# Performance work log

Measured on AMD Instinct MI355X. Metric: run time of the kernel, lower is better.

Reference implementation:

```python
import jax, jax.numpy as jnp
import numpy as np

NUM_SAMPLES = 2048
MAX_AGENTS = 64
D_MODEL = 128
NUM_HEADS = 8


def setup_inputs() -> dict:
    key = jax.random.key(0)
    # deterministic ragged sizes: 1..64 repeating -> total = 32 * (64*65/2) = 66560
    agents = ((np.arange(NUM_SAMPLES) % MAX_AGENTS) + 1).astype(np.int32)
    total = int(agents.sum())
    k1, k2, k3 = jax.random.split(key, 3)
    s = 1.0 / np.sqrt(D_MODEL)
    return {
        "att_in": jax.random.normal(k1, (total, D_MODEL), jnp.float32),
        "in_proj_w": jax.random.uniform(k2, (3 * D_MODEL, D_MODEL), jnp.float32, -s, s),
        "in_proj_b": jnp.zeros((3 * D_MODEL,), jnp.float32),
        "out_proj_w": jax.random.uniform(k3, (D_MODEL, D_MODEL), jnp.float32, -s, s),
        "out_proj_b": jnp.zeros((D_MODEL,), jnp.float32),
        "agents_per_sample": jnp.asarray(agents),
    }


def reference(att_in, in_proj_w, in_proj_b, out_proj_w, out_proj_b, agents_per_sample):
    # agents_per_sample is static ragged metadata (host ints)
    agents = np.asarray(agents_per_sample)
    B = len(agents)
    A = int(agents.max())
    D = att_in.shape[-1]
    hd = D // NUM_HEADS

    # scatter ragged tokens into zero-padded [B, A, D]
    sample_ids = np.repeat(np.arange(B), agents)
    pos = np.concatenate([np.arange(n) for n in agents])
    padded = jnp.zeros((B, A, D), att_in.dtype).at[sample_ids, pos].set(att_in)
    key_valid = jnp.asarray(np.arange(A)[None, :] < agents[:, None])  # [B, A]

    # torch nn.MultiheadAttention math (eval mode, dropout=0)
    qkv = padded @ in_proj_w.T + in_proj_b  # [B, A, 3D]
    q, k, v = jnp.split(qkv, 3, axis=-1)
    q = q.reshape(B, A, NUM_HEADS, hd)
    k = k.reshape(B, A, NUM_HEADS, hd)
    v = v.reshape(B, A, NUM_HEADS, hd)

    scores = jnp.einsum("bqhd,bkhd->bhqk", q, k) / jnp.sqrt(jnp.asarray(hd, q.dtype))
    scores = jnp.where(key_valid[:, None, None, :], scores, jnp.asarray(-1e30, scores.dtype))
    attn = jax.nn.softmax(scores, axis=-1)

    out = jnp.einsum("bhqk,bkhd->bqhd", attn, v).reshape(B, A, D)
    out = out @ out_proj_w.T + out_proj_b

    # unpad: concatenation of the per-sample ragged outputs
    return out[sample_ids, pos]
```

## Files before the change

### kernel.cpp

```cpp
#include <hip/hip_runtime.h>

#define DM 128
#define NHEADS 8

typedef __attribute__((ext_vector_type(8))) __bf16 bf16x8;
typedef __attribute__((ext_vector_type(8))) unsigned short u16x8;
typedef __attribute__((ext_vector_type(4))) float f32x4;

__device__ inline unsigned short f2bf(float f) {
    unsigned u = __float_as_uint(f);
    u += 0x7FFFu + ((u >> 16) & 1u);
    return (unsigned short)(u >> 16);
}

__global__ void prep(const int* __restrict__ agents, int B,
                     const float* __restrict__ wqkv, const float* __restrict__ wout,
                     int* __restrict__ offs,
                     unsigned short* __restrict__ wqkv_bf,
                     unsigned short* __restrict__ wout_bf) {
    if (blockIdx.x < 64) {
        int idx = (blockIdx.x * 256 + threadIdx.x) * 4;
        if (idx < 49152) {
            float4 v = *(const float4*)(wqkv + idx);
            ushort4 o;
            o.x = f2bf(v.x); o.y = f2bf(v.y); o.z = f2bf(v.z); o.w = f2bf(v.w);
            *(ushort4*)(wqkv_bf + idx) = o;
        } else {
            int j = idx - 49152;
            float4 v = *(const float4*)(wout + j);
            ushort4 o;
            o.x = f2bf(v.x); o.y = f2bf(v.y); o.z = f2bf(v.z); o.w = f2bf(v.w);
            *(ushort4*)(wout_bf + j) = o;
        }
    } else {
        __shared__ int part[256];
        const int tid = threadIdx.x;
        const int per = (B + 255) >> 8;
        const int base = tid * per;
        int s = 0;
        for (int i = 0; i < per; ++i) {
            int idx = base + i;
            if (idx < B) s += agents[idx];
        }
        part[tid] = s;
        __syncthreads();
        for (int off = 1; off < 256; off <<= 1) {
            int v = (tid >= off) ? part[tid - off] : 0;
            __syncthreads();
            part[tid] += v;
            __syncthreads();
        }
        int run = (tid == 0) ? 0 : part[tid - 1];
        for (int i = 0; i < per; ++i) {
            int idx = base + i;
            if (idx < B) { offs[idx] = run; run += agents[idx]; }
        }
    }
}

template<int NT>
__device__ __forceinline__ void fused_body(
    const unsigned short* __restrict__ wqkvb, const float* __restrict__ bqkv,
    const unsigned short* __restrict__ woutb, const float* __restrict__ bout,
    float* __restrict__ out,
    unsigned short* __restrict__ Xs, unsigned short* __restrict__ Vs,
    int n, int base, int h, int quad, int l16)
{
    constexpr int G   = (NT + 1) / 2;
    constexpr int KT2 = 2 * G;
    bf16x8 qf[NT], kf[NT];
    const int shA = (quad & 1) * 32 + l16;
    const int shB = shA + 16;

    #pragma unroll
    for (int seg = 0; seg < 3; ++seg) {
        bf16x8 wf[4];
        #pragma unroll
        for (int ks = 0; ks < 4; ++ks)
            wf[ks] = *(const bf16x8*)(wqkvb +
                     (size_t)(seg * 128 + h * 16 + l16) * 128 + ks * 32 + quad * 8);
        const float4 bs = *(const float4*)(bqkv + seg * 128 + h * 16 + quad * 4);
        #pragma unroll
        for (int mt = 0; mt < NT; ++mt) {
            f32x4 acc = {0.f, 0.f, 0.f, 0.f};
            #pragma unroll
            for (int ks = 0; ks < 4; ++ks) {
                bf16x8 xf = *(const bf16x8*)&Xs[(mt * 16 + l16) * 136 + ks * 32 + quad * 8];
                acc = __builtin_amdgcn_mfma_f32_16x16x32_bf16(wf[ks], xf, acc, 0, 0, 0);
            }
            ushort4 w;
            w.x = f2bf(acc[0] + bs.x); w.y = f2bf(acc[1] + bs.y);
            w.z = f2bf(acc[2] + bs.z); w.w = f2bf(acc[3] + bs.w);
            if (seg == 2) {
                *(ushort4*)&Vs[(mt * 16 + l16) * 136 + h * 16 + quad * 4] = w;
            } else {
                unsigned u0 = (unsigned)w.x | ((unsigned)w.y << 16);
                unsigned u1 = (unsigned)w.z | ((unsigned)w.w << 16);
                uint4 q;
                q.x = __shfl(u0, shA); q.y = __shfl(u1, shA);
                q.z = __shfl(u0, shB); q.w = __shfl(u1, shB);
                bf16x8 fr = (quad < 2) ? __builtin_bit_cast(bf16x8, q)
                                       : (bf16x8)(__bf16)0.0f;
                if (seg == 0) qf[mt] = fr; else kf[mt] = fr;
            }
        }
    }

    bf16x8 vA[G];
    const __bf16* Vsb = (const __bf16*)Vs;
    #pragma unroll
    for (int g = 0; g < G; ++g)
        #pragma unroll
        for (int j = 0; j < 8; ++j)
            vA[g][j] = Vsb[(size_t)(g * 32 + ((j >> 2) * 16) + quad * 4 + (j & 3)) * 136
                           + h * 16 + l16];

    __syncthreads();

    int thr[KT2];
    #pragma unroll
    for (int kt = 0; kt < KT2; ++kt) {
        int t = n - kt * 16 - quad * 4;
        thr[kt] = t < 0 ? 0 : (t > 4 ? 4 : t);
    }
    const float SC2 = 0.25f * 1.44269504088896340736f;
    unsigned short* Os = Xs;

    #pragma unroll
    for (int mt = 0; mt < NT; ++mt) {
        float pr[KT2][4];
        float mm = -3.0e38f;
        #pragma unroll
        for (int kt = 0; kt < KT2; ++kt) {
            if (kt < NT) {
                f32x4 sc = __builtin_amdgcn_mfma_f32_16x16x32_bf16(
                    kf[kt], qf[mt], (f32x4){0.f, 0.f, 0.f, 0.f}, 0, 0, 0);
                #pragma unroll
                for (int r = 0; r < 4; ++r) {
                    float v = sc[r] * SC2;
                    pr[kt][r] = v;
                    mm = fmaxf(mm, v);
                }
            } else {
                #pragma unroll
                for (int r = 0; r < 4; ++r) pr[kt][r] = -3.0e38f;
            }
        }
        mm = fmaxf(mm, __shfl_xor(mm, 16));
        mm = fmaxf(mm, __shfl_xor(mm, 32));
        float ll = 0.f;
        #pragma unroll
        for (int kt = 0; kt < KT2; ++kt)
            #pragma unroll
            for (int r = 0; r < 4; ++r) {
                float e = exp2f(pr[kt][r] - mm);
                e = (r < thr[kt]) ? e : 0.f;
                pr[kt][r] = e;
                ll += e;
            }
        ll += __shfl_xor(ll, 16);
        ll += __shfl_xor(ll, 32);
        float inv = __builtin_amdgcn_rcpf(ll);
        bf16x8 pf[G];
        #pragma unroll
        for (int g = 0; g < G; ++g)
            #pragma unroll
            for (int j = 0; j < 8; ++j)
                pf[g][j] = (__bf16)(pr[2 * g + (j >> 2)][j & 3] * inv);
        f32x4 o = __builtin_amdgcn_mfma_f32_16x16x32_bf16(
            vA[0], pf[0], (f32x4){0.f, 0.f, 0.f, 0.f}, 0, 0, 0);
        if constexpr (G == 2)
            o = __builtin_amdgcn_mfma_f32_16x16x32_bf16(vA[1], pf[1], o, 0, 0, 0);
        const int row = mt * 16 + l16;
        if (row < n) {
            ushort4 w;
            w.x = f2bf(o[0]); w.y = f2bf(o[1]); w.z = f2bf(o[2]); w.w = f2bf(o[3]);
            *(ushort4*)&Os[row * 136 + h * 16 + quad * 4] = w;
        }
    }
    __syncthreads();

    bf16x8 wf2[4];
    #pragma unroll
    for (int ks = 0; ks < 4; ++ks)
        wf2[ks] = *(const bf16x8*)(woutb +
                  (size_t)(h * 16 + l16) * 128 + ks * 32 + quad * 8);
    const float4 bo = *(const float4*)(bout + h * 16 + quad * 4);
    #pragma unroll
    for (int mt = 0; mt < NT; ++mt) {
        const int row = mt * 16 + l16;
        f32x4 acc = {0.f, 0.f, 0.f, 0.f};
        #pragma unroll
        for (int ks = 0; ks < 4; ++ks) {
            bf16x8 af = *(const bf16x8*)&Os[row * 136 + ks * 32 + quad * 8];
            acc = __builtin_amdgcn_mfma_f32_16x16x32_bf16(wf2[ks], af, acc, 0, 0, 0);
        }
        if (row < n) {
            float4 o;
            o.x = acc[0] + bo.x; o.y = acc[1] + bo.y;
            o.z = acc[2] + bo.z; o.w = acc[3] + bo.w;
            *(float4*)(out + (size_t)(base + row) * DM + h * 16 + quad * 4) = o;
        }
    }
}

#define XS_OFF 0
#define VS_OFF 17408
#define SMEMF  34816

__launch_bounds__(512, 4)
__global__ void fused(const float* __restrict__ x,
                      const unsigned short* __restrict__ wqkvb,
                      const float* __restrict__ bqkv,
                      const unsigned short* __restrict__ woutb,
                      const float* __restrict__ bout,
                      float* __restrict__ out,
                      const int* __restrict__ agents,
                      const int* __restrict__ offs) {
    __shared__ __align__(16) char smem[SMEMF];
    unsigned short* Xs = (unsigned short*)(smem + XS_OFF);
    unsigned short* Vs = (unsigned short*)(smem + VS_OFF);

    const int s = blockIdx.x;
    const int n = agents[s];
    const int base = offs[s];
    const int tid = threadIdx.x;
    const int h = tid >> 6, lane = tid & 63, quad = lane >> 4, l16 = lane & 15;

    for (int f = tid; f < 1088; f += 512)
        ((uint4*)(smem + VS_OFF))[f] = make_uint4(0u, 0u, 0u, 0u);
    for (int f = tid; f < 2048; f += 512) {
        int t = f >> 5, c = f & 31;
        ushort4 o = make_ushort4(0, 0, 0, 0);
        if (t < n) {
            float4 v = *(const float4*)(x + (size_t)(base + t) * DM + c * 4);
            o.x = f2bf(v.x); o.y = f2bf(v.y); o.z = f2bf(v.z); o.w = f2bf(v.w);
        }
        *(ushort4*)&Xs[t * 136 + c * 4] = o;
    }
    __syncthreads();

    const int nkt = (n + 15) >> 4;
    if      (nkt == 1) fused_body<1>(wqkvb, bqkv, woutb, bout, out, Xs, Vs, n, base, h, quad, l16);
    else if (nkt == 2) fused_body<2>(wqkvb, bqkv, woutb, bout, out, Xs, Vs, n, base, h, quad, l16);
    else if (nkt == 3) fused_body<3>(wqkvb, bqkv, woutb, bout, out, Xs, Vs, n, base, h, quad, l16);
    else               fused_body<4>(wqkvb, bqkv, woutb, bout, out, Xs, Vs, n, base, h, quad, l16);
}

extern "C" void kernel_launch(void* const* d_in, const int* in_sizes, int n_in,
                              void* d_out, int out_size, void* d_ws, size_t ws_size,
                              hipStream_t stream) {
    const float* att_in     = (const float*)d_in[0];
    const float* in_proj_w  = (const float*)d_in[1];
    const float* in_proj_b  = (const float*)d_in[2];
    const float* out_proj_w = (const float*)d_in[3];
    const float* out_proj_b = (const float*)d_in[4];
    const int*   agents     = (const int*)d_in[5];
    const int B = in_sizes[5];

    int* offs = (int*)d_ws;
    unsigned short* wqkv_bf = (unsigned short*)((char*)d_ws + 8192);
    unsigned short* wout_bf = (unsigned short*)((char*)d_ws + 106496);

    hipLaunchKernelGGL(prep, dim3(65), dim3(256), 0, stream,
                       agents, B, in_proj_w, out_proj_w, offs, wqkv_bf, wout_bf);
    hipLaunchKernelGGL(fused, dim3(B), dim3(512), 0, stream,
                       att_in, wqkv_bf, in_proj_b, wout_bf, out_proj_b,
                       (float*)d_out, agents, offs);
}
```

Measured before the change: 149.0 us.

## Split fused attention into bf16 pre-conversion, QKV-attention, and output-projection kernels

Moves the fp32-to-bf16 conversion of the input tokens into the prep kernel. The per-sample kernel now reads bf16 rows straight from global memory and keeps V in registers through a swapped-operand MFMA, so it needs no shared-memory staging. The attention output goes to a global bf16 buffer that reuses the input buffer in place. A separate tiled kernel then does the output projection with the weights staged in LDS. The aim is to cut LDS use and synchronisation in the per-sample kernel and to run the projection as a dense GEMM, at the cost of an extra launch and extra global round trips.

```diff
diff --git a/kernel.cpp b/kernel.cpp
--- a/kernel.cpp
+++ b/kernel.cpp
@@ -1,10 +1,8 @@
 #include <hip/hip_runtime.h>
 
 #define DM 128
-#define NHEADS 8
 
 typedef __attribute__((ext_vector_type(8))) __bf16 bf16x8;
-typedef __attribute__((ext_vector_type(8))) unsigned short u16x8;
 typedef __attribute__((ext_vector_type(4))) float f32x4;
 
 __device__ inline unsigned short f2bf(float f) {
@@ -13,11 +11,13 @@
     return (unsigned short)(u >> 16);
 }
 
-__global__ void prep(const int* __restrict__ agents, int B,
+__global__ void prep(const int* __restrict__ agents, int B, int M,
                      const float* __restrict__ wqkv, const float* __restrict__ wout,
+                     const float* __restrict__ x,
                      int* __restrict__ offs,
                      unsigned short* __restrict__ wqkv_bf,
-                     unsigned short* __restrict__ wout_bf) {
+                     unsigned short* __restrict__ wout_bf,
+                     unsigned short* __restrict__ xbf) {
     if (blockIdx.x < 64) {
         int idx = (blockIdx.x * 256 + threadIdx.x) * 4;
         if (idx < 49152) {
@@ -32,7 +32,7 @@
             o.x = f2bf(v.x); o.y = f2bf(v.y); o.z = f2bf(v.z); o.w = f2bf(v.w);
             *(ushort4*)(wout_bf + j) = o;
         }
-    } else {
+    } else if (blockIdx.x == 64) {
         __shared__ int part[256];
         const int tid = threadIdx.x;
         const int per = (B + 255) >> 8;
@@ -55,25 +55,38 @@
             int idx = base + i;
             if (idx < B) { offs[idx] = run; run += agents[idx]; }
         }
+    } else {
+        const int nf4 = M * 32;
+        const int stride = ((int)gridDim.x - 65) * 256;
+        for (int idx = ((int)blockIdx.x - 65) * 256 + (int)threadIdx.x; idx < nf4;
+             idx += stride) {
+            float4 v = ((const float4*)x)[idx];
+            ushort4 o;
+            o.x = f2bf(v.x); o.y = f2bf(v.y); o.z = f2bf(v.z); o.w = f2bf(v.w);
+            ((ushort4*)xbf)[idx] = o;
+        }
     }
 }
 
 template<int NT>
-__device__ __forceinline__ void fused_body(
-    const unsigned short* __restrict__ wqkvb, const float* __restrict__ bqkv,
-    const unsigned short* __restrict__ woutb, const float* __restrict__ bout,
-    float* __restrict__ out,
-    unsigned short* __restrict__ Xs, unsigned short* __restrict__ Vs,
-    int n, int base, int h, int quad, int l16)
+__device__ __forceinline__ void qa_body(
+    const unsigned short* __restrict__ xbf,
+    const unsigned short* __restrict__ wqkvb,
+    const float* __restrict__ bqkv,
+    unsigned short* __restrict__ obuf,
+    int n, int base, int M, int h, int quad, int l16)
 {
     constexpr int G   = (NT + 1) / 2;
     constexpr int KT2 = 2 * G;
-    bf16x8 qf[NT], kf[NT];
+    bf16x8 qf[NT], kf[NT], vA[G];
+    #pragma unroll
+    for (int g = 0; g < G; ++g) vA[g] = (bf16x8)(__bf16)0.0f;
+
     const int shA = (quad & 1) * 32 + l16;
     const int shB = shA + 16;
 
     #pragma unroll
-    for (int seg = 0; seg < 3; ++seg) {
+    for (int seg = 0; seg < 2; ++seg) {
         bf16x8 wf[4];
         #pragma unroll
         for (int ks = 0; ks < 4; ++ks)
@@ -82,38 +95,51 @@
         const float4 bs = *(const float4*)(bqkv + seg * 128 + h * 16 + quad * 4);
         #pragma unroll
         for (int mt = 0; mt < NT; ++mt) {
+            int row = base + mt * 16 + l16;
+            row = row < M ? row : M - 1;
+            const unsigned short* xr = xbf + (size_t)row * 128;
             f32x4 acc = {0.f, 0.f, 0.f, 0.f};
             #pragma unroll
             for (int ks = 0; ks < 4; ++ks) {
-                bf16x8 xf = *(const bf16x8*)&Xs[(mt * 16 + l16) * 136 + ks * 32 + quad * 8];
+                bf16x8 xf = *(const bf16x8*)(xr + ks * 32 + quad * 8);
                 acc = __builtin_amdgcn_mfma_f32_16x16x32_bf16(wf[ks], xf, acc, 0, 0, 0);
             }
             ushort4 w;
             w.x = f2bf(acc[0] + bs.x); w.y = f2bf(acc[1] + bs.y);
             w.z = f2bf(acc[2] + bs.z); w.w = f2bf(acc[3] + bs.w);
-            if (seg == 2) {
-                *(ushort4*)&Vs[(mt * 16 + l16) * 136 + h * 16 + quad * 4] = w;
-            } else {
-                unsigned u0 = (unsigned)w.x | ((unsigned)w.y << 16);
-                unsigned u1 = (unsigned)w.z | ((unsigned)w.w << 16);
-                uint4 q;
-                q.x = __shfl(u0, shA); q.y = __shfl(u1, shA);
-                q.z = __shfl(u0, shB); q.w = __shfl(u1, shB);
-                bf16x8 fr = (quad < 2) ? __builtin_bit_cast(bf16x8, q)
-                                       : (bf16x8)(__bf16)0.0f;
-                if (seg == 0) qf[mt] = fr; else kf[mt] = fr;
+            unsigned u0 = (unsigned)w.x | ((unsigned)w.y << 16);
+            unsigned u1 = (unsigned)w.z | ((unsigned)w.w << 16);
+            uint4 q;
+            q.x = __shfl(u0, shA); q.y = __shfl(u1, shA);
+            q.z = __shfl(u0, shB); q.w = __shfl(u1, shB);
+            bf16x8 fr = (quad < 2) ? __builtin_bit_cast(bf16x8, q)
+                                   : (bf16x8)(__bf16)0.0f;
+            if (seg == 0) qf[mt] = fr; else kf[mt] = fr;
+        }
+    }
+    {
+        bf16x8 wfv[4];
+        #pragma unroll
+        for (int ks = 0; ks < 4; ++ks)
+            wfv[ks] = *(const bf16x8*)(wqkvb +
+                      (size_t)(256 + h * 16 + l16) * 128 + ks * 32 + quad * 8);
+        const float bv = bqkv[256 + h * 16 + l16];
+        #pragma unroll
+        for (int t = 0; t < NT; ++t) {
+            int row = base + t * 16 + l16;
+            row = row < M ? row : M - 1;
+            const unsigned short* xr = xbf + (size_t)row * 128;
+            f32x4 acc = {0.f, 0.f, 0.f, 0.f};
+            #pragma unroll
+            for (int ks = 0; ks < 4; ++ks) {
+                bf16x8 xf = *(const bf16x8*)(xr + ks * 32 + quad * 8);
+                acc = __builtin_amdgcn_mfma_f32_16x16x32_bf16(xf, wfv[ks], acc, 0, 0, 0);
             }
-        }
-    }
-
-    bf16x8 vA[G];
-    const __bf16* Vsb = (const __bf16*)Vs;
-    #pragma unroll
-    for (int g = 0; g < G; ++g)
-        #pragma unroll
-        for (int j = 0; j < 8; ++j)
-            vA[g][j] = Vsb[(size_t)(g * 32 + ((j >> 2) * 16) + quad * 4 + (j & 3)) * 136
-                           + h * 16 + l16];
+            #pragma unroll
+            for (int r = 0; r < 4; ++r)
+                vA[t >> 1][(t & 1) * 4 + r] = (__bf16)(acc[r] + bv);
+        }
+    }
 
     __syncthreads();
 
@@ -124,7 +150,6 @@
         thr[kt] = t < 0 ? 0 : (t > 4 ? 4 : t);
     }
     const float SC2 = 0.25f * 1.44269504088896340736f;
-    unsigned short* Os = Xs;
 
     #pragma unroll
     for (int mt = 0; mt < NT; ++mt) {
@@ -175,76 +200,78 @@
         if (row < n) {
             ushort4 w;
             w.x = f2bf(o[0]); w.y = f2bf(o[1]); w.z = f2bf(o[2]); w.w = f2bf(o[3]);
-            *(ushort4*)&Os[row * 136 + h * 16 + quad * 4] = w;
-        }
-    }
-    __syncthreads();
-
-    bf16x8 wf2[4];
-    #pragma unroll
-    for (int ks = 0; ks < 4; ++ks)
-        wf2[ks] = *(const bf16x8*)(woutb +
-                  (size_t)(h * 16 + l16) * 128 + ks * 32 + quad * 8);
-    const float4 bo = *(const float4*)(bout + h * 16 + quad * 4);
-    #pragma unroll
-    for (int mt = 0; mt < NT; ++mt) {
-        const int row = mt * 16 + l16;
-        f32x4 acc = {0.f, 0.f, 0.f, 0.f};
-        #pragma unroll
-        for (int ks = 0; ks < 4; ++ks) {
-            bf16x8 af = *(const bf16x8*)&Os[row * 136 + ks * 32 + quad * 8];
-            acc = __builtin_amdgcn_mfma_f32_16x16x32_bf16(wf2[ks], af, acc, 0, 0, 0);
-        }
-        if (row < n) {
-            float4 o;
-            o.x = acc[0] + bo.x; o.y = acc[1] + bo.y;
-            o.z = acc[2] + bo.z; o.w = acc[3] + bo.w;
-            *(float4*)(out + (size_t)(base + row) * DM + h * 16 + quad * 4) = o;
-        }
-    }
-}
-
-#define XS_OFF 0
-#define VS_OFF 17408
-#define SMEMF  34816
-
-__launch_bounds__(512, 4)
-__global__ void fused(const float* __restrict__ x,
-                      const unsigned short* __restrict__ wqkvb,
-                      const float* __restrict__ bqkv,
-                      const unsigned short* __restrict__ woutb,
-                      const float* __restrict__ bout,
-                      float* __restrict__ out,
-                      const int* __restrict__ agents,
-                      const int* __restrict__ offs) {
-    __shared__ __align__(16) char smem[SMEMF];
-    unsigned short* Xs = (unsigned short*)(smem + XS_OFF);
-    unsigned short* Vs = (unsigned short*)(smem + VS_OFF);
-
+            *(ushort4*)(obuf + (size_t)(base + row) * 128 + h * 16 + quad * 4) = w;
+        }
+    }
+}
+
+__launch_bounds__(512, 2)
+__global__ void qkvattn(const unsigned short* __restrict__ xbf,
+                        const unsigned short* __restrict__ wqkvb,
+                        const float* __restrict__ bqkv,
+                        unsigned short* __restrict__ obuf,
+                        const int* __restrict__ agents,
+                        const int* __restrict__ offs,
+                        int M) {
     const int s = blockIdx.x;
     const int n = agents[s];
     const int base = offs[s];
     const int tid = threadIdx.x;
-    const int h = tid >> 6, lane = tid & 63, quad = lane >> 4, l16 = lane & 15;
-
-    for (int f = tid; f < 1088; f += 512)
-        ((uint4*)(smem + VS_OFF))[f] = make_uint4(0u, 0u, 0u, 0u);
-    for (int f = tid; f < 2048; f += 512) {
-        int t = f >> 5, c = f & 31;
-        ushort4 o = make_ushort4(0, 0, 0, 0);
-        if (t < n) {
-            float4 v = *(const float4*)(x + (size_t)(base + t) * DM + c * 4);
-            o.x = f2bf(v.x); o.y = f2bf(v.y); o.z = f2bf(v.z); o.w = f2bf(v.w);
-        }
-        *(ushort4*)&Xs[t * 136 + c * 4] = o;
-    }
+    const int h = tid >> 6, quad = (tid >> 4) & 3, l16 = tid & 15;
+    const int nt = (n + 15) >> 4;
+    if      (nt == 1) qa_body<1>(xbf, wqkvb, bqkv, obuf, n, base, M, h, quad, l16);
+    else if (nt == 2) qa_body<2>(xbf, wqkvb, bqkv, obuf, n, base, M, h, quad, l16);
+    else if (nt == 3) qa_body<3>(xbf, wqkvb, bqkv, obuf, n, base, M, h, quad, l16);
+    else              qa_body<4>(xbf, wqkvb, bqkv, obuf, n, base, M, h, quad, l16);
+}
+
+__launch_bounds__(256, 4)
+__global__ void oproj(const unsigned short* __restrict__ attn_b,
+                      const unsigned short* __restrict__ woutb,
+                      const float* __restrict__ bout,
+                      float* __restrict__ out, int M) {
+    __shared__ __align__(16) unsigned short Ws[128 * 136];
+    __shared__ __align__(16) float biass[128];
+    const int m0 = blockIdx.x * 64;
+    const int tid = threadIdx.x;
+
+    for (int f = tid; f < 2048; f += 256) {
+        int t = f >> 4, c = f & 15;
+        *(uint4*)&Ws[t * 136 + c * 8] = *(const uint4*)(woutb + (size_t)t * 128 + c * 8);
+    }
+    if (tid < 32)
+        ((float4*)biass)[tid] = ((const float4*)bout)[tid];
     __syncthreads();
 
-    const int nkt = (n + 15) >> 4;
-    if      (nkt == 1) fused_body<1>(wqkvb, bqkv, woutb, bout, out, Xs, Vs, n, base, h, quad, l16);
-    else if (nkt == 2) fused_body<2>(wqkvb, bqkv, woutb, bout, out, Xs, Vs, n, base, h, quad, l16);
-    else if (nkt == 3) fused_body<3>(wqkvb, bqkv, woutb, bout, out, Xs, Vs, n, base, h, quad, l16);
-    else               fused_body<4>(wqkvb, bqkv, woutb, bout, out, Xs, Vs, n, base, h, quad, l16);
+    const int wave = tid >> 6, lane = tid & 63, quad = lane >> 4, l16 = lane & 15;
+    const int mw = m0 + wave * 16;
+
+    bf16x8 af[4];
+    {
+        int row = mw + l16;
+        row = (row < M) ? row : (M - 1);
+        #pragma unroll
+        for (int ks = 0; ks < 4; ++ks)
+            af[ks] = *(const bf16x8*)(attn_b + (size_t)row * DM + ks * 32 + quad * 8);
+    }
+
+    const int row0 = mw + l16;
+
+    for (int ct = 0; ct < 8; ++ct) {
+        bf16x8 bc[4];
+        #pragma unroll
+        for (int ks = 0; ks < 4; ++ks)
+            bc[ks] = *(const bf16x8*)&Ws[(ct * 16 + l16) * 136 + ks * 32 + quad * 8];
+        f32x4 a0 = {0.f, 0.f, 0.f, 0.f};
+        #pragma unroll
+        for (int ks = 0; ks < 4; ++ks)
+            a0 = __builtin_amdgcn_mfma_f32_16x16x32_bf16(bc[ks], af[ks], a0, 0, 0, 0);
+        const int n0 = ct * 16 + quad * 4;
+        const float4 b4 = *(const float4*)(biass + n0);
+        float4 o0;
+        o0.x = a0[0] + b4.x; o0.y = a0[1] + b4.y; o0.z = a0[2] + b4.z; o0.w = a0[3] + b4.w;
+        if (row0 < M) *(float4*)(out + (size_t)row0 * DM + n0) = o0;
+    }
 }
 
 extern "C" void kernel_launch(void* const* d_in, const int* in_sizes, int n_in,
@@ -257,14 +284,18 @@
     const float* out_proj_b = (const float*)d_in[4];
     const int*   agents     = (const int*)d_in[5];
     const int B = in_sizes[5];
+    const int M = out_size / DM;
 
     int* offs = (int*)d_ws;
     unsigned short* wqkv_bf = (unsigned short*)((char*)d_ws + 8192);
     unsigned short* wout_bf = (unsigned short*)((char*)d_ws + 106496);
-
-    hipLaunchKernelGGL(prep, dim3(65), dim3(256), 0, stream,
-                       agents, B, in_proj_w, out_proj_w, offs, wqkv_bf, wout_bf);
-    hipLaunchKernelGGL(fused, dim3(B), dim3(512), 0, stream,
-                       att_in, wqkv_bf, in_proj_b, wout_bf, out_proj_b,
-                       (float*)d_out, agents, offs);
-}
+    unsigned short* xobuf   = (unsigned short*)((char*)d_ws + 139264);
+
+    hipLaunchKernelGGL(prep, dim3(65 + 1024), dim3(256), 0, stream,
+                       agents, B, M, in_proj_w, out_proj_w, att_in,
+                       offs, wqkv_bf, wout_bf, xobuf);
+    hipLaunchKernelGGL(qkvattn, dim3(B), dim3(512), 0, stream,
+                       xobuf, wqkv_bf, in_proj_b, xobuf, agents, offs, M);
+    hipLaunchKernelGGL(oproj, dim3((M + 63) / 64), dim3(256), 0, stream,
+                       xobuf, wout_bf, out_proj_b, (float*)d_out, M);
+}
```

Measured after the change: 170.7 us. 14.5% more time.
